# Kernel tuning notes

Measured on AMD Instinct MI355X. Metric: run time of the kernel, lower is better.

The kernel has to match this reference:

```python
import jax, jax.numpy as jnp
import numpy as np

B, N, M = 32, 32, 64          # batch, timesteps, local group length (group_token_length+3)
NL, NG = 192, 768             # n_embd_local, n_embd_global
HL, HG = 6, 12                # n_head_local, n_head_global


def setup_inputs() -> dict:
    key = jax.random.key(0)
    ks = jax.random.split(key, 16)
    def w(k, shape, s=0.02):
        return jax.random.normal(k, shape, jnp.float32) * s
    inp = {}
    inp["xl"] = jax.random.normal(ks[0], (B, N, M, NL), jnp.float32)
    inp["xg"] = jax.random.normal(ks[1], (B, 2 * N, NG), jnp.float32)
    i = 2
    for pre, d in (("l", NL), ("g", NG)):
        inp[f"{pre}_ln1_w"] = jnp.ones((d,), jnp.float32)
        inp[f"{pre}_ln1_b"] = jnp.zeros((d,), jnp.float32)
        inp[f"{pre}_ln2_w"] = jnp.ones((d,), jnp.float32)
        inp[f"{pre}_ln2_b"] = jnp.zeros((d,), jnp.float32)
        for nm in ("q", "k", "v", "o"):
            inp[f"{pre}_w{nm}"] = w(ks[i], (d, d)); i += 1
            inp[f"{pre}_b{nm}"] = jnp.zeros((d,), jnp.float32)
        inp[f"{pre}_w1"] = w(ks[i], (d, 4 * d)); i += 1
        inp[f"{pre}_b1"] = jnp.zeros((4 * d,), jnp.float32)
        inp[f"{pre}_w2"] = w(ks[i], (4 * d, d)); i += 1
        inp[f"{pre}_b2"] = jnp.zeros((d,), jnp.float32)
    inp["d_w"] = w(ks[i], (M * NL, NG))
    inp["d_b"] = jnp.zeros((NG,), jnp.float32)
    return inp


def _ln(x, g, b):
    m = x.mean(-1, keepdims=True)
    v = ((x - m) ** 2).mean(-1, keepdims=True)
    return (x - m) / jnp.sqrt(v + 1e-5) * g + b


def _attn(x, wq, bq, wk, bk, wv, bv, wo, bo, nh, allow):
    # x: [B', L, D]; allow: [L, L] bool (True = attend)
    Bx, L, D = x.shape
    hd = D // nh
    q = (x @ wq + bq).reshape(Bx, L, nh, hd)
    k = (x @ wk + bk).reshape(Bx, L, nh, hd)
    v = (x @ wv + bv).reshape(Bx, L, nh, hd)
    s = jnp.einsum('bihd,bjhd->bhij', q, k) / np.float32(np.sqrt(hd))
    s = jnp.where(allow[None, None], s, -jnp.inf)
    p = jax.nn.softmax(s, axis=-1)
    y = jnp.einsum('bhij,bjhd->bihd', p, v).reshape(Bx, L, D)
    return y @ wo + bo


def _tblock(x, p, nh, allow):
    (ln1w, ln1b, ln2w, ln2b, wq, bq, wk, bk, wv, bv, wo, bo, w1, b1, w2, b2) = p
    x = x + _attn(_ln(x, ln1w, ln1b), wq, bq, wk, bk, wv, bv, wo, bo, nh, allow)
    h = _ln(x, ln2w, ln2b)
    return x + (jax.nn.gelu(h @ w1 + b1, approximate=False) @ w2 + b2)


def reference(xl, xg,
              l_ln1_w, l_ln1_b, l_ln2_w, l_ln2_b,
              l_wq, l_bq, l_wk, l_bk, l_wv, l_bv, l_wo, l_bo,
              l_w1, l_b1, l_w2, l_b2,
              g_ln1_w, g_ln1_b, g_ln2_w, g_ln2_b,
              g_wq, g_bq, g_wk, g_bk, g_wv, g_bv, g_wo, g_bo,
              g_w1, g_b1, g_w2, g_b2,
              d_w, d_b):
    Bx, Nx, Mx, nl = xl.shape
    ng = xg.shape[-1]
    lp = (l_ln1_w, l_ln1_b, l_ln2_w, l_ln2_b, l_wq, l_bq, l_wk, l_bk,
          l_wv, l_bv, l_wo, l_bo, l_w1, l_b1, l_w2, l_b2)
    gp = (g_ln1_w, g_ln1_b, g_ln2_w, g_ln2_b, g_wq, g_bq, g_wk, g_bk,
          g_wv, g_bv, g_wo, g_bo, g_w1, g_b1, g_w2, g_b2)

    # local block: causal attention within each group of M tokens
    allow_l = jnp.tril(jnp.ones((Mx, Mx), bool))
    x = _tblock(xl.reshape(Bx * Nx, Mx, nl), lp, HL, allow_l)
    xl_out = x.reshape(Bx, Nx, Mx, nl)

    # summarize each group into one global token, interleave with xg pairs
    zg = (xl_out.reshape(Bx, Nx, Mx * nl) @ d_w + d_b)[:, :, None, :]  # [B,N,1,ng]
    zg = jnp.concatenate([zg, xg.reshape(Bx, Nx, 2, ng)], axis=2)      # [B,N,3,ng]
    zg = zg.reshape(Bx, 3 * Nx, ng)

    # global mask: tril plus within-triplet upper entries; the global block
    # additionally applies its own causal mask, so combined = causal & custom
    L = 3 * Nx
    idx = jnp.arange(L)
    causal = idx[:, None] >= idx[None, :]
    custom = causal | (idx[:, None] // 3 == idx[None, :] // 3)
    allow_g = causal & custom

    zg = _tblock(zg, gp, HG, allow_g)
    xg_out = zg.reshape(Bx, Nx, 3, ng)[:, :, 1:, :].reshape(Bx, 2 * Nx, ng)
    return (xl_out, xg_out)
```

## Files before the change

### kernel.cpp

```cpp
#include <hip/hip_runtime.h>
#include <hip/hip_bf16.h>


typedef unsigned short ushort;
typedef __bf16 bf16x8 __attribute__((ext_vector_type(8)));
typedef float f32x4 __attribute__((ext_vector_type(4)));

__device__ __forceinline__ ushort f2us(float f) {
  __hip_bfloat16 h = __float2bfloat16(f);
  return *reinterpret_cast<ushort*>(&h);
}
__device__ __forceinline__ float gelu_exact(float v) {
  return 0.5f * v * (1.f + erff(v * 0.70710678118654752f));
}
__device__ __forceinline__ void gload16(const ushort* g, ushort* l) {
  __builtin_amdgcn_global_load_lds(
      (const __attribute__((address_space(1))) void*)g,
      (__attribute__((address_space(3))) void*)l, 16, 0, 0);
}

struct TJobs { const float* s[13]; ushort* d[13]; };

__global__ __launch_bounds__(256)
void transp_all(TJobs J)
{
  static constexpr int NN[13]  = {192,192,192,192,768,192,768,768,768,768,768,3072,768};
  static constexpr int SS[13]  = {192,192,192,192,192,768,12288,768,768,768,768,768,3072};
  static constexpr int RO[13]  = {0,192,384,0,0,0,0,0,768,1536,0,0,0};
  static constexpr int CUM[14] = {0,9,18,27,36,72,108,2412,2556,2700,2844,2988,3564,4140};
  __shared__ float t[64][65];
  int bid = blockIdx.x;
  int j = 0;
  while (bid >= CUM[j + 1]) ++j;
  int tIdx = bid - CUM[j];
  const int N = NN[j], stride = SS[j], rowOff = RO[j];
  const int nx = N >> 6;
  const int n0 = (tIdx % nx) * 64, k0 = (tIdx / nx) * 64;
  const float* W = J.s[j];
  ushort* Wt = J.d[j];
  int c = threadIdx.x & 63, r = threadIdx.x >> 6;
  #pragma unroll
  for (int i = 0; i < 16; ++i) {
    int kr = r + i * 4;
    t[kr][c] = W[(size_t)(k0 + kr) * N + n0 + c];
  }
  __syncthreads();
  #pragma unroll
  for (int i = 0; i < 16; ++i) {
    int nr = r + i * 4;
    Wt[(size_t)(rowOff + n0 + nr) * stride + k0 + c] = f2us(t[c][nr]);
  }
}

__global__ __launch_bounds__(256)
void pack3_kernel(float* dst, const float* a, int na, const float* b, int nb,
                  const float* c, int nc)
{
  int i = blockIdx.x * 256 + threadIdx.x;
  if (i >= na + nb + nc) return;
  dst[i] = (i < na) ? a[i] : (i < na + nb ? b[i - na] : c[i - na - nb]);
}

template<int D>
__global__ __launch_bounds__(256)
void ln_kernel(const float* __restrict__ x, const float* __restrict__ g,
               const float* __restrict__ bb, ushort* __restrict__ out, int rows)
{
  int wave = threadIdx.x >> 6, lane = threadIdx.x & 63;
  int row = blockIdx.x * 4 + wave;
  if (row >= rows) return;
  const float* xr = x + (size_t)row * D;
  constexpr int E = D / 64;
  float vals[E];
  float s = 0.f;
  #pragma unroll
  for (int e = 0; e < E; ++e) { vals[e] = xr[e * 64 + lane]; s += vals[e]; }
  #pragma unroll
  for (int off = 32; off >= 1; off >>= 1) s += __shfl_xor(s, off);
  float m = s * (1.f / D);
  float s2 = 0.f;
  #pragma unroll
  for (int e = 0; e < E; ++e) { float d = vals[e] - m; s2 += d * d; }
  #pragma unroll
  for (int off = 32; off >= 1; off >>= 1) s2 += __shfl_xor(s2, off);
  float rstd = rsqrtf(s2 * (1.f / D) + 1e-5f);
  ushort* orow = out + (size_t)row * D;
  #pragma unroll
  for (int e = 0; e < E; ++e) {
    int c = e * 64 + lane;
    orow[c] = f2us((vals[e] - m) * rstd * g[c] + bb[c]);
  }
}

__global__ __launch_bounds__(256, 2)
void fused_mlp(const ushort* __restrict__ A, const ushort* __restrict__ W1t,
               const ushort* __restrict__ W2t, const float* __restrict__ b1,
               const float* __restrict__ b2, const float* __restrict__ resF,
               float* __restrict__ Cf, ushort* __restrict__ Cb)
{
  __shared__ __align__(16) ushort Hs[64 * 72];
  const int tid = threadIdx.x;
  const int wave = tid >> 6, lane = tid & 63;
  const int quad = lane >> 4, lm = lane & 15;
  const int rowBase = blockIdx.x * 64;
  const int wr  = (wave & 1) * 32;
  const int wc1 = (wave >> 1) * 32;
  const int wc2 = (wave >> 1) * 96;

  bf16x8 afr[2][6];
  #pragma unroll
  for (int r2 = 0; r2 < 2; ++r2)
    #pragma unroll
    for (int kt = 0; kt < 6; ++kt)
      afr[r2][kt] = *reinterpret_cast<const bf16x8*>(
          &A[(size_t)(rowBase + wr + r2 * 16 + lm) * 192 + kt * 32 + quad * 8]);

  f32x4 acc2[2][6] = {};
  for (int ht = 0; ht < 12; ++ht) {
    f32x4 acc1[2][2] = {};
    #pragma unroll
    for (int kt = 0; kt < 6; ++kt) {
      bf16x8 bfr[2];
      #pragma unroll
      for (int c2 = 0; c2 < 2; ++c2)
        bfr[c2] = *reinterpret_cast<const bf16x8*>(
            &W1t[(size_t)(ht * 64 + wc1 + c2 * 16 + lm) * 192 + kt * 32 + quad * 8]);
      #pragma unroll
      for (int r2 = 0; r2 < 2; ++r2)
        #pragma unroll
        for (int c2 = 0; c2 < 2; ++c2)
          acc1[r2][c2] = __builtin_amdgcn_mfma_f32_16x16x32_bf16(
              afr[r2][kt], bfr[c2], acc1[r2][c2], 0, 0, 0);
    }
    __syncthreads();
    #pragma unroll
    for (int r2 = 0; r2 < 2; ++r2)
      #pragma unroll
      for (int c2 = 0; c2 < 2; ++c2) {
        int col = wc1 + c2 * 16 + lm;
        float bb1 = b1[ht * 64 + col];
        #pragma unroll
        for (int g = 0; g < 4; ++g) {
          int row = wr + r2 * 16 + quad * 4 + g;
          Hs[row * 72 + col] = f2us(gelu_exact(acc1[r2][c2][g] + bb1));
        }
      }
    __syncthreads();
    #pragma unroll
    for (int s = 0; s < 2; ++s) {
      bf16x8 ap[2], bp[6];
      #pragma unroll
      for (int r2 = 0; r2 < 2; ++r2)
        ap[r2] = *reinterpret_cast<const bf16x8*>(
            &Hs[(wr + r2 * 16 + lm) * 72 + s * 32 + quad * 8]);
      #pragma unroll
      for (int c2 = 0; c2 < 6; ++c2)
        bp[c2] = *reinterpret_cast<const bf16x8*>(
            &W2t[(size_t)(wc2 + c2 * 16 + lm) * 768 + ht * 64 + s * 32 + quad * 8]);
      #pragma unroll
      for (int r2 = 0; r2 < 2; ++r2)
        #pragma unroll
        for (int c2 = 0; c2 < 6; ++c2)
          acc2[r2][c2] = __builtin_amdgcn_mfma_f32_16x16x32_bf16(
              ap[r2], bp[c2], acc2[r2][c2], 0, 0, 0);
    }
  }
  #pragma unroll
  for (int r2 = 0; r2 < 2; ++r2)
    #pragma unroll
    for (int c2 = 0; c2 < 6; ++c2) {
      int col = wc2 + c2 * 16 + lm;
      float bb2 = b2[col];
      #pragma unroll
      for (int g = 0; g < 4; ++g) {
        int row = rowBase + wr + r2 * 16 + quad * 4 + g;
        size_t idx = (size_t)row * 192 + col;
        float v = acc2[r2][c2][g] + bb2 + resF[idx];
        Cf[idx] = v;
        Cb[idx] = f2us(v);
      }
    }
}

template<int ACT, int RES, int OUTF, int OUTB, int BIAS>
__global__ __launch_bounds__(256)
void mgemm(const ushort* __restrict__ A, const ushort* __restrict__ Bt,
           const float* __restrict__ bias, const float* __restrict__ resF,
           float* __restrict__ Cf, ushort* __restrict__ Cb,
           int M, int N, int K)
{
  __shared__ __align__(16) ushort Asm[2][128 * 32];
  __shared__ __align__(16) ushort Bsm[2][64 * 32];
  const int tid = threadIdx.x;
  const int wave = tid >> 6, lane = tid & 63;
  const int quad = lane >> 4, lm = lane & 15;
  const int rowBase = blockIdx.y * 128, colBase = blockIdx.x * 64;
  const int wrow = (wave & 1) * 64, wcol = (wave >> 1) * 32;
  const int srow = lane >> 2, skcol = (lane & 3) * 8;
  const int nIter = K >> 5;

  auto stage = [&](int buf, int it) {
    const int k0 = it * 32;
    #pragma unroll
    for (int uu = 0; uu < 3; ++uu) {
      const int u = wave * 3 + uu;
      if (u < 8) {
        const ushort* gp = A + (size_t)(rowBase + u * 16 + srow) * K + k0 + skcol;
        gload16(gp, &Asm[buf][u * 512]);
      } else {
        const int v = u - 8;
        const ushort* gp = Bt + (size_t)(colBase + v * 16 + srow) * K + k0 + skcol;
        gload16(gp, &Bsm[buf][v * 512]);
      }
    }
  };

  f32x4 acc[4][2] = {};
  stage(0, 0);
  if (nIter > 1) stage(1, 1);

  for (int t = 0; t < nIter; ++t) {
    const int cur = t & 1;
    if (t + 1 < nIter) asm volatile("s_waitcnt vmcnt(3)" ::: "memory");
    else               asm volatile("s_waitcnt vmcnt(0)" ::: "memory");
    __builtin_amdgcn_s_barrier();
    bf16x8 af[4], bfr[2];
    #pragma unroll
    for (int r2 = 0; r2 < 4; ++r2)
      af[r2] = *reinterpret_cast<const bf16x8*>(&Asm[cur][(wrow + r2 * 16 + lm) * 32 + quad * 8]);
    #pragma unroll
    for (int c2 = 0; c2 < 2; ++c2)
      bfr[c2] = *reinterpret_cast<const bf16x8*>(&Bsm[cur][(wcol + c2 * 16 + lm) * 32 + quad * 8]);
    asm volatile("s_waitcnt lgkmcnt(0)" ::: "memory");
    __builtin_amdgcn_s_barrier();
    if (t + 2 < nIter) stage(cur, t + 2);
    #pragma unroll
    for (int r2 = 0; r2 < 4; ++r2)
      #pragma unroll
      for (int c2 = 0; c2 < 2; ++c2)
        acc[r2][c2] = __builtin_amdgcn_mfma_f32_16x16x32_bf16(af[r2], bfr[c2], acc[r2][c2], 0, 0, 0);
  }

  #pragma unroll
  for (int r2 = 0; r2 < 4; ++r2) {
    #pragma unroll
    for (int c2 = 0; c2 < 2; ++c2) {
      int col = colBase + wcol + c2 * 16 + lm;
      int row0 = rowBase + wrow + r2 * 16 + quad * 4;
      #pragma unroll
      for (int g = 0; g < 4; ++g) {
        float v = acc[r2][c2][g];
        size_t idx = (size_t)(row0 + g) * N + col;
        if (BIAS) v += bias[col];
        if (ACT == 1) v = gelu_exact(v);
        if (RES) v += resF[idx];
        if (OUTF) Cf[idx] = v;
        if (OUTB) Cb[idx] = f2us(v);
      }
    }
  }
}

template<int ACT, int RES, int OUTF, int OUTB, int BIAS, int SPLITK>
__global__ __launch_bounds__(256)
void mgemm128(const ushort* __restrict__ A, const ushort* __restrict__ Bt,
              const float* __restrict__ bias, const float* __restrict__ resF,
              float* __restrict__ Cf, ushort* __restrict__ Cb,
              int M, int N, int K, int kChunk)
{
  __shared__ __align__(16) ushort Asm[2][128 * 32];
  __shared__ __align__(16) ushort Bsm[2][128 * 32];
  const int tid = threadIdx.x;
  const int wave = tid >> 6, lane = tid & 63;
  const int quad = lane >> 4, lm = lane & 15;
  const int rowBase = blockIdx.y * 128, colBase = blockIdx.x * 128;
  const int wrow = (wave & 1) * 64, wcol = (wave >> 1) * 64;
  const int srow = lane >> 2, skcol = (lane & 3) * 8;

  const int kbeg = SPLITK ? blockIdx.z * kChunk : 0;
  const int nIter = (SPLITK ? kChunk : K) >> 5;

  auto stage = [&](int buf, int it) {
    const int k0 = kbeg + it * 32;
    #pragma unroll
    for (int uu = 0; uu < 4; ++uu) {
      const int u = wave * 4 + uu;
      if (u < 8) {
        const ushort* gp = A + (size_t)(rowBase + u * 16 + srow) * K + k0 + skcol;
        gload16(gp, &Asm[buf][u * 512]);
      } else {
        const int v = u - 8;
        const ushort* gp = Bt + (size_t)(colBase + v * 16 + srow) * K + k0 + skcol;
        gload16(gp, &Bsm[buf][v * 512]);
      }
    }
  };

  f32x4 acc[4][4] = {};
  stage(0, 0);
  if (nIter > 1) stage(1, 1);

  for (int t = 0; t < nIter; ++t) {
    const int cur = t & 1;
    if (t + 1 < nIter) asm volatile("s_waitcnt vmcnt(4)" ::: "memory");
    else               asm volatile("s_waitcnt vmcnt(0)" ::: "memory");
    __builtin_amdgcn_s_barrier();
    bf16x8 af[4], bfr[4];
    #pragma unroll
    for (int r2 = 0; r2 < 4; ++r2)
      af[r2] = *reinterpret_cast<const bf16x8*>(&Asm[cur][(wrow + r2 * 16 + lm) * 32 + quad * 8]);
    #pragma unroll
    for (int c2 = 0; c2 < 4; ++c2)
      bfr[c2] = *reinterpret_cast<const bf16x8*>(&Bsm[cur][(wcol + c2 * 16 + lm) * 32 + quad * 8]);
    asm volatile("s_waitcnt lgkmcnt(0)" ::: "memory");
    __builtin_amdgcn_s_barrier();
    if (t + 2 < nIter) stage(cur, t + 2);
    #pragma unroll
    for (int r2 = 0; r2 < 4; ++r2)
      #pragma unroll
      for (int c2 = 0; c2 < 4; ++c2)
        acc[r2][c2] = __builtin_amdgcn_mfma_f32_16x16x32_bf16(af[r2], bfr[c2], acc[r2][c2], 0, 0, 0);
  }

  const size_t zoff = SPLITK ? (size_t)blockIdx.z * M * N : 0;
  #pragma unroll
  for (int r2 = 0; r2 < 4; ++r2) {
    #pragma unroll
    for (int c2 = 0; c2 < 4; ++c2) {
      int col = colBase + wcol + c2 * 16 + lm;
      int row0 = rowBase + wrow + r2 * 16 + quad * 4;
      #pragma unroll
      for (int g = 0; g < 4; ++g) {
        float v = acc[r2][c2][g];
        size_t idx = (size_t)(row0 + g) * N + col;
        if (BIAS) v += bias[col];
        if (ACT == 1) v = gelu_exact(v);
        if (RES) v += resF[idx];
        if (OUTF) Cf[zoff + idx] = v;
        if (OUTB) Cb[idx] = f2us(v);
      }
    }
  }
}

__global__ __launch_bounds__(256)
void reduce8_kernel(const float* __restrict__ P, const float* __restrict__ db,
                    float* __restrict__ ZG)
{
  int i = blockIdx.x * 256 + threadIdx.x;
  float s = db[i % 768];
  #pragma unroll
  for (int k = 0; k < 8; ++k) s += P[i + k * 786432];
  ZG[i] = s;
}

__global__ __launch_bounds__(256)
void reduce4res_kernel(const float* __restrict__ P, const float* __restrict__ db,
                       const float* __restrict__ res, float* __restrict__ out)
{
  int i = blockIdx.x * 256 + threadIdx.x;
  float s = db[i % 768] + res[i];
  #pragma unroll
  for (int k = 0; k < 4; ++k) s += P[i + k * 2359296];
  out[i] = s;
}

template<int L, int HD, int NW>
__global__ __launch_bounds__(NW * 64)
void fattn(const ushort* __restrict__ QKV, ushort* __restrict__ Yp,
           int nh, int DS, int DY, int offQ, int offK, int offV)
{
  constexpr int PQ = HD + 8;
  constexpr int PV = L + 8;
  constexpr int KS = HD / 32;
  constexpr int NCT = L / 16;
  constexpr int KS2 = L / 32;
  constexpr int NYT = HD / 16;
  constexpr int T = NW * 64;
  __shared__ __align__(16) ushort Ql[L * PQ];
  __shared__ __align__(16) ushort Kl[L * PQ];
  __shared__ __align__(16) ushort Vt[HD * PV];
  __shared__ __align__(16) ushort Ps[L * PV];
  const int tid = threadIdx.x;
  const int b = blockIdx.x / nh, h = blockIdx.x % nh;
  const size_t rowb = (size_t)b * L * DS;
  const int hb = h * HD;
  constexpr int CH = L * HD / 8;
  for (int idx = tid; idx < CH; idx += T) {
    int row = idx / (HD / 8), seg = idx % (HD / 8);
    uint4 q4 = *reinterpret_cast<const uint4*>(&QKV[rowb + (size_t)row * DS + offQ + hb + seg * 8]);
    *reinterpret_cast<uint4*>(&Ql[row * PQ + seg * 8]) = q4;
    uint4 k4 = *reinterpret_cast<const uint4*>(&QKV[rowb + (size_t)row * DS + offK + hb + seg * 8]);
    *reinterpret_cast<uint4*>(&Kl[row * PQ + seg * 8]) = k4;
  }
  for (int idx = tid; idx < L * HD; idx += T) {
    int j = idx / HD, d = idx % HD;
    Vt[d * PV + j] = QKV[rowb + (size_t)j * DS + offV + hb + d];
  }
  __syncthreads();
  const int lane = tid & 63;
  const int quad = lane >> 4, lm = lane & 15;
  const int rt = tid >> 6;
  const float scale = rsqrtf((float)HD);
  bf16x8 af[KS];
  #pragma unroll
  for (int s = 0; s < KS; ++s)
    af[s] = *reinterpret_cast<const bf16x8*>(&Ql[(rt * 16 + lm) * PQ + s * 32 + quad * 8]);
  f32x4 sacc[NCT] = {};
  #pragma unroll
  for (int ct = 0; ct < NCT; ++ct)
    #pragma unroll
    for (int s = 0; s < KS; ++s) {
      bf16x8 bf = *reinterpret_cast<const bf16x8*>(&Kl[(ct * 16 + lm) * PQ + s * 32 + quad * 8]);
      sacc[ct] = __builtin_amdgcn_mfma_f32_16x16x32_bf16(af[s], bf, sacc[ct], 0, 0, 0);
    }
  float inv[4];
  #pragma unroll
  for (int g = 0; g < 4; ++g) {
    const int row = rt * 16 + quad * 4 + g;
    float sv[NCT]; float m = -1e30f;
    #pragma unroll
    for (int ct = 0; ct < NCT; ++ct) {
      int col = ct * 16 + lm;
      float x = sacc[ct][g] * scale;
      sv[ct] = (col <= row) ? x : -1e30f;
      m = fmaxf(m, sv[ct]);
    }
    #pragma unroll
    for (int off = 8; off >= 1; off >>= 1) m = fmaxf(m, __shfl_xor(m, off));
    float l = 0.f;
    #pragma unroll
    for (int ct = 0; ct < NCT; ++ct) {
      float p = __expf(sv[ct] - m);
      l += p;
      Ps[row * PV + ct * 16 + lm] = f2us(p);
    }
    #pragma unroll
    for (int off = 8; off >= 1; off >>= 1) l += __shfl_xor(l, off);
    inv[g] = 1.f / l;
  }
  __syncthreads();
  f32x4 yacc[NYT] = {};
  #pragma unroll
  for (int s = 0; s < KS2; ++s) {
    bf16x8 ap = *reinterpret_cast<const bf16x8*>(&Ps[(rt * 16 + lm) * PV + s * 32 + quad * 8]);
    #pragma unroll
    for (int ct = 0; ct < NYT; ++ct) {
      bf16x8 bv = *reinterpret_cast<const bf16x8*>(&Vt[(ct * 16 + lm) * PV + s * 32 + quad * 8]);
      yacc[ct] = __builtin_amdgcn_mfma_f32_16x16x32_bf16(ap, bv, yacc[ct], 0, 0, 0);
    }
  }
  #pragma unroll
  for (int ct = 0; ct < NYT; ++ct)
    #pragma unroll
    for (int g = 0; g < 4; ++g) {
      int row = rt * 16 + quad * 4 + g;
      int d = ct * 16 + lm;
      Yp[((size_t)b * L + row) * DY + hb + d] = f2us(yacc[ct][g] * inv[g]);
    }
}

__global__ __launch_bounds__(256)
void interleave_kernel(const float* __restrict__ zg, const float* __restrict__ xg,
                       float* __restrict__ z)
{
  int idx = blockIdx.x * 256 + threadIdx.x;
  int c = idx % 768;
  int tok = idx / 768;
  int b = tok / 96, r = tok % 96;
  int n = r / 3, t = r % 3;
  z[idx] = (t == 0) ? zg[((size_t)b * 32 + n) * 768 + c]
                    : xg[((size_t)b * 64 + 2 * n + (t - 1)) * 768 + c];
}

__global__ __launch_bounds__(256)
void gather_kernel(const float* __restrict__ zfin, float* __restrict__ dst)
{
  int idx = blockIdx.x * 256 + threadIdx.x;
  int c = idx % 768;
  int t = (idx / 768) % 64;
  int b = idx / (768 * 64);
  int n = t >> 1, s = t & 1;
  dst[idx] = zfin[((size_t)b * 96 + 3 * n + 1 + s) * 768 + c];
}

extern "C" void kernel_launch(void* const* d_in, const int* in_sizes, int n_in,
                              void* d_out, int out_size, void* d_ws, size_t ws_size,
                              hipStream_t stream) {
  const float* xl = (const float*)d_in[0];
  const float* xg = (const float*)d_in[1];
  const float* l_ln1_w = (const float*)d_in[2];  const float* l_ln1_b = (const float*)d_in[3];
  const float* l_ln2_w = (const float*)d_in[4];  const float* l_ln2_b = (const float*)d_in[5];
  const float* l_wq = (const float*)d_in[6];     const float* l_bq = (const float*)d_in[7];
  const float* l_wk = (const float*)d_in[8];     const float* l_bk = (const float*)d_in[9];
  const float* l_wv = (const float*)d_in[10];    const float* l_bv = (const float*)d_in[11];
  const float* l_wo = (const float*)d_in[12];    const float* l_bo = (const float*)d_in[13];
  const float* l_w1 = (const float*)d_in[14];    const float* l_b1 = (const float*)d_in[15];
  const float* l_w2 = (const float*)d_in[16];    const float* l_b2 = (const float*)d_in[17];
  const float* g_ln1_w = (const float*)d_in[18]; const float* g_ln1_b = (const float*)d_in[19];
  const float* g_ln2_w = (const float*)d_in[20]; const float* g_ln2_b = (const float*)d_in[21];
  const float* g_wq = (const float*)d_in[22];    const float* g_bq = (const float*)d_in[23];
  const float* g_wk = (const float*)d_in[24];    const float* g_bk = (const float*)d_in[25];
  const float* g_wv = (const float*)d_in[26];    const float* g_bv = (const float*)d_in[27];
  const float* g_wo = (const float*)d_in[28];    const float* g_bo = (const float*)d_in[29];
  const float* g_w1 = (const float*)d_in[30];    const float* g_b1 = (const float*)d_in[31];
  const float* g_w2 = (const float*)d_in[32];    const float* g_b2 = (const float*)d_in[33];
  const float* dw   = (const float*)d_in[34];    const float* db   = (const float*)d_in[35];

  float* outL = (float*)d_out;
  float* outG = outL + 12582912;

  char* W = (char*)d_ws;
  ushort* A_bf   = (ushort*)(W + 0);
  ushort* QKVl   = (ushort*)(W + 25165824);
  ushort* XLb    = (ushort*)(W + 75497472);
  float*  X1     = (float*)(W + 100663296);
  ushort* wqkv_t = (ushort*)(W + 150994944);
  ushort* wo_t   = (ushort*)(W + 151216128);
  ushort* w1_t   = (ushort*)(W + 151289856);
  ushort* w2_t   = (ushort*)(W + 151584768);
  ushort* wd_t   = (ushort*)(W + 151879680);
  ushort* wgqkv_t= (ushort*)(W + 170754048);
  ushort* wgo_t  = (ushort*)(W + 174292992);
  ushort* wg1_t  = (ushort*)(W + 175472640);
  ushort* wg2_t  = (ushort*)(W + 180191232);
  float*  bqkv_l = (float*)(W + 184909824);
  float*  bqkv_g = (float*)(W + 184912128);
  float*  ZGP  = (float*)(W + 0);
  float*  FC2P = (float*)(W + 0);
  float*  ZG   = (float*)(W + 25165824);
  float*  Z    = (float*)(W + 28311552);
  ushort* LNG  = (ushort*)(W + 37748736);
  ushort* QKVg = (ushort*)(W + 42467328);
  ushort* YG   = (ushort*)(W + 56623104);
  float*  X1G  = (float*)(W + 61341696);
  ushort* HLNG = (ushort*)(W + 70778880);
  ushort* HIDg = (ushort*)(W + 100663296);
  float*  OUTG = (float*)(W + 119537664);

  TJobs tj;
  tj.s[0] = l_wq; tj.s[1] = l_wk; tj.s[2] = l_wv; tj.s[3] = l_wo;
  tj.s[4] = l_w1; tj.s[5] = l_w2; tj.s[6] = dw;
  tj.s[7] = g_wq; tj.s[8] = g_wk; tj.s[9] = g_wv; tj.s[10] = g_wo;
  tj.s[11] = g_w1; tj.s[12] = g_w2;
  tj.d[0] = wqkv_t; tj.d[1] = wqkv_t; tj.d[2] = wqkv_t; tj.d[3] = wo_t;
  tj.d[4] = w1_t; tj.d[5] = w2_t; tj.d[6] = wd_t;
  tj.d[7] = wgqkv_t; tj.d[8] = wgqkv_t; tj.d[9] = wgqkv_t; tj.d[10] = wgo_t;
  tj.d[11] = wg1_t; tj.d[12] = wg2_t;
  transp_all<<<4140, 256, 0, stream>>>(tj);
  pack3_kernel<<<3, 256, 0, stream>>>(bqkv_l, l_bq, 192, l_bk, 192, l_bv, 192);
  pack3_kernel<<<9, 256, 0, stream>>>(bqkv_g, g_bq, 768, g_bk, 768, g_bv, 768);

  ln_kernel<192><<<16384, 256, 0, stream>>>(xl, l_ln1_w, l_ln1_b, A_bf, 65536);
  mgemm<0,0,0,1,1><<<dim3(9,512), 256, 0, stream>>>(A_bf, wqkv_t, bqkv_l, nullptr, nullptr, QKVl, 65536, 576, 192);
  fattn<64,32,4><<<6144, 256, 0, stream>>>(QKVl, A_bf, 6, 576, 192, 0, 192, 384);
  mgemm<0,1,1,0,1><<<dim3(3,512), 256, 0, stream>>>(A_bf, wo_t, l_bo, xl, X1, nullptr, 65536, 192, 192);
  ln_kernel<192><<<16384, 256, 0, stream>>>(X1, l_ln2_w, l_ln2_b, A_bf, 65536);
  fused_mlp<<<1024, 256, 0, stream>>>(A_bf, w1_t, w2_t, l_b1, l_b2, X1, outL, XLb);
  mgemm128<0,0,1,0,0,1><<<dim3(6,8,8), 256, 0, stream>>>(XLb, wd_t, nullptr, nullptr, ZGP, nullptr, 1024, 768, 12288, 1536);
  reduce8_kernel<<<3072, 256, 0, stream>>>(ZGP, db, ZG);
  interleave_kernel<<<9216, 256, 0, stream>>>(ZG, xg, Z);
  ln_kernel<768><<<768, 256, 0, stream>>>(Z, g_ln1_w, g_ln1_b, LNG, 3072);
  mgemm128<0,0,0,1,1,0><<<dim3(18,24), 256, 0, stream>>>(LNG, wgqkv_t, bqkv_g, nullptr, nullptr, QKVg, 3072, 2304, 768, 0);
  fattn<96,64,6><<<384, 384, 0, stream>>>(QKVg, YG, 12, 2304, 768, 0, 768, 1536);
  mgemm<0,1,1,0,1><<<dim3(12,24), 256, 0, stream>>>(YG, wgo_t, g_bo, Z, X1G, nullptr, 3072, 768, 768);
  ln_kernel<768><<<768, 256, 0, stream>>>(X1G, g_ln2_w, g_ln2_b, HLNG, 3072);
  mgemm128<1,0,0,1,1,0><<<dim3(24,24), 256, 0, stream>>>(HLNG, wg1_t, g_b1, nullptr, nullptr, HIDg, 3072, 3072, 768, 0);
  mgemm128<0,0,1,0,0,1><<<dim3(6,24,4), 256, 0, stream>>>(HIDg, wg2_t, nullptr, nullptr, FC2P, nullptr, 3072, 768, 3072, 768);
  reduce4res_kernel<<<9216, 256, 0, stream>>>(FC2P, g_b2, X1G, OUTG);
  gather_kernel<<<6144, 256, 0, stream>>>(OUTG, outG);
}
```

Baseline: 699.0 us.

## Restructure local fused MLP to materialize full hidden row tile in LDS

The local fused MLP kernel now handles 32 rows per block instead of 64. It computes the whole 768-wide GELU hidden tile into shared memory in one pass, with each wave covering 192 hidden columns. It then runs the second GEMM over the full K with a single barrier, instead of interleaving 12 hidden chunks with two barriers each. This removes repeated synchronization and gives each wave a narrower output slice, but it doubles the grid, halves the reuse of W1/W2 per block, and uses about 48KB of LDS, which may limit occupancy.

New measurement: 696.4 us. No clear change (-0.4%).

```diff
diff --git a/kernel.cpp b/kernel.cpp
--- a/kernel.cpp
+++ b/kernel.cpp
@@ -98,82 +98,77 @@
                const float* __restrict__ b2, const float* __restrict__ resF,
                float* __restrict__ Cf, ushort* __restrict__ Cb)
 {
-  __shared__ __align__(16) ushort Hs[64 * 72];
+  constexpr int PH = 776;
+  __shared__ __align__(16) ushort Hsf[32 * PH];
   const int tid = threadIdx.x;
   const int wave = tid >> 6, lane = tid & 63;
   const int quad = lane >> 4, lm = lane & 15;
-  const int rowBase = blockIdx.x * 64;
-  const int wr  = (wave & 1) * 32;
-  const int wc1 = (wave >> 1) * 32;
-  const int wc2 = (wave >> 1) * 96;
-
-  bf16x8 afr[2][6];
-  #pragma unroll
-  for (int r2 = 0; r2 < 2; ++r2)
-    #pragma unroll
-    for (int kt = 0; kt < 6; ++kt)
-      afr[r2][kt] = *reinterpret_cast<const bf16x8*>(
-          &A[(size_t)(rowBase + wr + r2 * 16 + lm) * 192 + kt * 32 + quad * 8]);
-
-  f32x4 acc2[2][6] = {};
-  for (int ht = 0; ht < 12; ++ht) {
-    f32x4 acc1[2][2] = {};
-    #pragma unroll
-    for (int kt = 0; kt < 6; ++kt) {
-      bf16x8 bfr[2];
-      #pragma unroll
-      for (int c2 = 0; c2 < 2; ++c2)
-        bfr[c2] = *reinterpret_cast<const bf16x8*>(
-            &W1t[(size_t)(ht * 64 + wc1 + c2 * 16 + lm) * 192 + kt * 32 + quad * 8]);
+  const int rowBase = blockIdx.x * 32;
+
+  {
+    bf16x8 afr[2][6];
+    #pragma unroll
+    for (int r2 = 0; r2 < 2; ++r2)
+      #pragma unroll
+      for (int kt = 0; kt < 6; ++kt)
+        afr[r2][kt] = *reinterpret_cast<const bf16x8*>(
+            &A[(size_t)(rowBase + r2 * 16 + lm) * 192 + kt * 32 + quad * 8]);
+
+    const int cb = wave * 192;
+    #pragma unroll
+    for (int ct = 0; ct < 12; ++ct) {
+      const int col = cb + ct * 16 + lm;
+      f32x4 acc1[2] = {};
+      #pragma unroll
+      for (int kt = 0; kt < 6; ++kt) {
+        bf16x8 bfr = *reinterpret_cast<const bf16x8*>(
+            &W1t[(size_t)col * 192 + kt * 32 + quad * 8]);
+        #pragma unroll
+        for (int r2 = 0; r2 < 2; ++r2)
+          acc1[r2] = __builtin_amdgcn_mfma_f32_16x16x32_bf16(
+              afr[r2][kt], bfr, acc1[r2], 0, 0, 0);
+      }
+      float bb1 = b1[col];
       #pragma unroll
       for (int r2 = 0; r2 < 2; ++r2)
         #pragma unroll
-        for (int c2 = 0; c2 < 2; ++c2)
-          acc1[r2][c2] = __builtin_amdgcn_mfma_f32_16x16x32_bf16(
-              afr[r2][kt], bfr[c2], acc1[r2][c2], 0, 0, 0);
-    }
-    __syncthreads();
+        for (int g = 0; g < 4; ++g) {
+          int row = r2 * 16 + quad * 4 + g;
+          Hsf[row * PH + col] = f2us(gelu_exact(acc1[r2][g] + bb1));
+        }
+    }
+  }
+  __syncthreads();
+
+  const int ob = wave * 48;
+  f32x4 acc2[2][3] = {};
+  #pragma unroll
+  for (int ks = 0; ks < 24; ++ks) {
+    bf16x8 ap[2], bp[3];
     #pragma unroll
     for (int r2 = 0; r2 < 2; ++r2)
-      #pragma unroll
-      for (int c2 = 0; c2 < 2; ++c2) {
-        int col = wc1 + c2 * 16 + lm;
-        float bb1 = b1[ht * 64 + col];
-        #pragma unroll
-        for (int g = 0; g < 4; ++g) {
-          int row = wr + r2 * 16 + quad * 4 + g;
-          Hs[row * 72 + col] = f2us(gelu_exact(acc1[r2][c2][g] + bb1));
-        }
-      }
-    __syncthreads();
-    #pragma unroll
-    for (int s = 0; s < 2; ++s) {
-      bf16x8 ap[2], bp[6];
-      #pragma unroll
-      for (int r2 = 0; r2 < 2; ++r2)
-        ap[r2] = *reinterpret_cast<const bf16x8*>(
-            &Hs[(wr + r2 * 16 + lm) * 72 + s * 32 + quad * 8]);
-      #pragma unroll
-      for (int c2 = 0; c2 < 6; ++c2)
-        bp[c2] = *reinterpret_cast<const bf16x8*>(
-            &W2t[(size_t)(wc2 + c2 * 16 + lm) * 768 + ht * 64 + s * 32 + quad * 8]);
-      #pragma unroll
-      for (int r2 = 0; r2 < 2; ++r2)
-        #pragma unroll
-        for (int c2 = 0; c2 < 6; ++c2)
-          acc2[r2][c2] = __builtin_amdgcn_mfma_f32_16x16x32_bf16(
-              ap[r2], bp[c2], acc2[r2][c2], 0, 0, 0);
-    }
+      ap[r2] = *reinterpret_cast<const bf16x8*>(
+          &Hsf[(r2 * 16 + lm) * PH + ks * 32 + quad * 8]);
+    #pragma unroll
+    for (int c2 = 0; c2 < 3; ++c2)
+      bp[c2] = *reinterpret_cast<const bf16x8*>(
+          &W2t[(size_t)(ob + c2 * 16 + lm) * 768 + ks * 32 + quad * 8]);
+    #pragma unroll
+    for (int r2 = 0; r2 < 2; ++r2)
+      #pragma unroll
+      for (int c2 = 0; c2 < 3; ++c2)
+        acc2[r2][c2] = __builtin_amdgcn_mfma_f32_16x16x32_bf16(
+            ap[r2], bp[c2], acc2[r2][c2], 0, 0, 0);
   }
   #pragma unroll
   for (int r2 = 0; r2 < 2; ++r2)
     #pragma unroll
-    for (int c2 = 0; c2 < 6; ++c2) {
-      int col = wc2 + c2 * 16 + lm;
+    for (int c2 = 0; c2 < 3; ++c2) {
+      int col = ob + c2 * 16 + lm;
       float bb2 = b2[col];
       #pragma unroll
       for (int g = 0; g < 4; ++g) {
-        int row = rowBase + wr + r2 * 16 + quad * 4 + g;
+        int row = rowBase + r2 * 16 + quad * 4 + g;
         size_t idx = (size_t)row * 192 + col;
         float v = acc2[r2][c2][g] + bb2 + resF[idx];
         Cf[idx] = v;
@@ -556,7 +551,7 @@
   fattn<64,32,4><<<6144, 256, 0, stream>>>(QKVl, A_bf, 6, 576, 192, 0, 192, 384);
   mgemm<0,1,1,0,1><<<dim3(3,512), 256, 0, stream>>>(A_bf, wo_t, l_bo, xl, X1, nullptr, 65536, 192, 192);
   ln_kernel<192><<<16384, 256, 0, stream>>>(X1, l_ln2_w, l_ln2_b, A_bf, 65536);
-  fused_mlp<<<1024, 256, 0, stream>>>(A_bf, w1_t, w2_t, l_b1, l_b2, X1, outL, XLb);
+  fused_mlp<<<2048, 256, 0, stream>>>(A_bf, w1_t, w2_t, l_b1, l_b2, X1, outL, XLb);
   mgemm128<0,0,1,0,0,1><<<dim3(6,8,8), 256, 0, stream>>>(XLb, wd_t, nullptr, nullptr, ZGP, nullptr, 1024, 768, 12288, 1536);
   reduce8_kernel<<<3072, 256, 0, stream>>>(ZGP, db, ZG);
   interleave_kernel<<<9216, 256, 0, stream>>>(ZG, xg, Z);
```
